# Kernel optimization log

Hardware: AMD Instinct MI355X
Metric: run time of the kernel (lower is better)

## Reference

```python
import jax, jax.numpy as jnp
import numpy as np

# Static options from the deep-stabilization repo
WIDTH, HEIGHT = 1920.0, 1080.0
NUM_GRID_ROWS = 12
FOV = 0.8  # virtual-camera vertical field of view (radians)


def quat_to_rotmat(q):
    """Quaternion (x, y, z, w) -> rotation matrix; q: [..., 4] -> [..., 3, 3]."""
    q = q / jnp.linalg.norm(q, axis=-1, keepdims=True)
    x, y, z, w = q[..., 0], q[..., 1], q[..., 2], q[..., 3]
    R = jnp.stack([
        1 - 2 * (y * y + z * z), 2 * (x * y - z * w), 2 * (x * z + y * w),
        2 * (x * y + z * w), 1 - 2 * (x * x + z * z), 2 * (y * z - x * w),
        2 * (x * z - y * w), 2 * (y * z + x * w), 1 - 2 * (x * x + y * y)
    ], axis=-1)
    return R.reshape(q.shape[:-1] + (3, 3))


def intrinsics():
    f = 0.5 * HEIGHT / np.tan(0.5 * FOV)
    return jnp.array([[f, 0.0, 0.5 * WIDTH],
                      [0.0, f, 0.5 * HEIGHT],
                      [0.0, 0.0, 1.0]], dtype=jnp.float32)


def setup_inputs() -> dict:
    key = jax.random.key(0)
    k1, k2 = jax.random.split(key)
    B = 1_048_576
    # Virtual camera quaternions [B, 4]
    Vt = jax.random.normal(k1, (B, 4), dtype=jnp.float32)
    # Real projections per grid row: K @ R(q) so they are valid, well-conditioned
    # projection matrices [B, NUM_GRID_ROWS, 3, 3]
    q = jax.random.normal(k2, (B, NUM_GRID_ROWS, 4), dtype=jnp.float32)
    Rr = quat_to_rotmat(q)
    real_projection_t = jnp.einsum('ij,brjk->brik', intrinsics(), Rr)
    return {"Vt": Vt, "real_projection_t": real_projection_t}


def reference(Vt, real_projection_t):
    K = intrinsics()
    # Virtual projection: K @ R(quat)  -> [B, 3, 3]
    Pv = jnp.einsum('ij,bjk->bik', K, quat_to_rotmat(Vt))
    # Real projection at the middle grid row -> [B, 3, 3]
    Pr = real_projection_t[:, NUM_GRID_ROWS // 2]
    # Homography from virtual frame to real frame
    transform = jnp.matmul(Pr, jnp.linalg.inv(Pv))  # [B, 3, 3]

    x0, x1 = int(WIDTH * 0.1), int(WIDTH * 0.9)
    y0, y1 = int(HEIGHT * 0.1), int(HEIGHT * 0.9)
    corners = jnp.array([[x0, y0, 1.0], [x0, y1, 1.0],
                         [x1, y0, 1.0], [x1, y1, 1.0]], dtype=jnp.float32)  # [4,3]

    pts = jnp.einsum('bij,cj->bci', transform, corners)  # [B, 4, 3]
    pts = pts / pts[..., 2:3]                            # homogeneous normalize
    xy = pts[..., :2] / jnp.array([WIDTH, HEIGHT], dtype=jnp.float32)  # [B,4,2]

    # Piecewise penalty |d|: d = x if x<0, 1-x if x>1, else 0  =>  relu(-x)+relu(x-1)
    viol = jax.nn.relu(-xy) + jax.nn.relu(xy - 1.0)  # [B, 4, 2]
    per_corner = viol.sum(axis=-1)                   # [B, 4]
    loss = per_corner.max(axis=-1).sum()             # max over corners, sum over batch
    return loss.reshape(1)
```

## Files before the change

kernel.cpp:

```cpp
#include <hip/hip_runtime.h>
#include <cmath>


__global__ __launch_bounds__(256) void loss_kernel(
    const float* __restrict__ Vt,
    const float* __restrict__ Prt,
    float* __restrict__ out,
    int B,
    float d0x, float d0y, float d1x, float d1y,
    float d2x, float d2y, float d3x, float d3y)
{
    int b = blockIdx.x * blockDim.x + threadIdx.x;
    float loss = 0.0f;
    if (b < B) {
        float4 q4 = *reinterpret_cast<const float4*>(Vt + 4ll * b);
        float qx = q4.x, qy = q4.y, qz = q4.z, qw = q4.w;
        float n  = sqrtf(qx*qx + qy*qy + qz*qz + qw*qw);
        float in_ = 1.0f / n;
        qx *= in_; qy *= in_; qz *= in_; qw *= in_;
        float r00 = 1.0f - 2.0f*(qy*qy + qz*qz);
        float r01 = 2.0f*(qx*qy - qz*qw);
        float r02 = 2.0f*(qx*qz + qy*qw);
        float r10 = 2.0f*(qx*qy + qz*qw);
        float r11 = 1.0f - 2.0f*(qx*qx + qz*qz);
        float r12 = 2.0f*(qy*qz - qx*qw);
        float r20 = 2.0f*(qx*qz - qy*qw);
        float r21 = 2.0f*(qy*qz + qx*qw);
        float r22 = 1.0f - 2.0f*(qx*qx + qy*qy);

        const float* P = Prt + (size_t)b * 108 + 54;
        float2 a0 = *reinterpret_cast<const float2*>(P + 0);
        float2 a1 = *reinterpret_cast<const float2*>(P + 2);
        float2 a2 = *reinterpret_cast<const float2*>(P + 4);
        float2 a3 = *reinterpret_cast<const float2*>(P + 6);
        float  p8 = P[8];
        float P0=a0.x, P1=a0.y, P2=a1.x, P3=a1.y, P4=a2.x, P5=a2.y, P6=a3.x, P7=a3.y, P8=p8;

        float m00 = P0*r00 + P1*r01 + P2*r02;
        float m01 = P0*r10 + P1*r11 + P2*r12;
        float m02 = P0*r20 + P1*r21 + P2*r22;
        float m10 = P3*r00 + P4*r01 + P5*r02;
        float m11 = P3*r10 + P4*r11 + P5*r12;
        float m12 = P3*r20 + P4*r21 + P5*r22;
        float m20 = P6*r00 + P7*r01 + P8*r02;
        float m21 = P6*r10 + P7*r11 + P8*r12;
        float m22 = P6*r20 + P7*r21 + P8*r22;

        const float invW = 1.0f / 1920.0f, invH = 1.0f / 1080.0f;
        float best = -1e30f;
        float dxs[4] = {d0x, d1x, d2x, d3x};
        float dys[4] = {d0y, d1y, d2y, d3y};
        #pragma unroll
        for (int c = 0; c < 4; ++c) {
            float dx = dxs[c], dy = dys[c];
            float px = m00*dx + m01*dy + m02;
            float py = m10*dx + m11*dy + m12;
            float pz = m20*dx + m21*dy + m22;
            float rz = 1.0f / pz;
            float x  = px * rz * invW;
            float y  = py * rz * invH;
            float v  = fmaxf(0.0f, -x) + fmaxf(0.0f, x - 1.0f)
                     + fmaxf(0.0f, -y) + fmaxf(0.0f, y - 1.0f);
            best = fmaxf(best, v);
        }
        loss = best;
    }

    #pragma unroll
    for (int off = 32; off > 0; off >>= 1)
        loss += __shfl_down(loss, off, 64);
    __shared__ float smem[4];
    int lane = threadIdx.x & 63;
    int wv   = threadIdx.x >> 6;
    if (lane == 0) smem[wv] = loss;
    __syncthreads();
    if (threadIdx.x == 0) {
        float s = smem[0] + smem[1] + smem[2] + smem[3];
        atomicAdd(out, s);
    }
}

extern "C" void kernel_launch(void* const* d_in, const int* in_sizes, int n_in,
                              void* d_out, int out_size, void* d_ws, size_t ws_size,
                              hipStream_t stream) {
    const float* Vt  = (const float*)d_in[0];
    const float* Prt = (const float*)d_in[1];
    float* out = (float*)d_out;
    int B = in_sizes[0] / 4;

    const double fd = 0.5 * 1080.0 / tan(0.5 * 0.8);
    const float  f  = (float)fd;
    const float  cx = 0.5f * 1920.0f, cy = 0.5f * 1080.0f;
    const float  x0 = 192.0f, x1 = 1728.0f, y0 = 108.0f, y1 = 972.0f;
    float d0x = (x0 - cx) / f, d0y = (y0 - cy) / f;
    float d1x = (x0 - cx) / f, d1y = (y1 - cy) / f;
    float d2x = (x1 - cx) / f, d2y = (y0 - cy) / f;
    float d3x = (x1 - cx) / f, d3y = (y1 - cy) / f;

    hipMemsetAsync(d_out, 0, sizeof(float), stream);
    int threads = 256;
    int blocks  = (B + threads - 1) / threads;
    loss_kernel<<<blocks, threads, 0, stream>>>(Vt, Prt, out, B,
        d0x, d0y, d1x, d1y, d2x, d2y, d3x, d3y);
}
```

Baseline: 531.5 us.

## Stage middle-row projections through LDS with coalesced aligned float4 loads

Each block of 256 records now loads the 16-byte-aligned 64-byte sections that contain the middle-row 3x3 matrices. It does this for groups of 4 records using cooperative float4 loads, writes them into a padded shared-memory stage, and each thread then reads its 9 floats from LDS at a fixed offset. The goal is to replace the strided, unaligned float2/float loads from a 432-byte record stride with fewer, wider, better-coalesced memory transactions. The cost is extra LDS traffic and a barrier, and a tail path that falls back to direct global loads for partial blocks.

```diff
diff --git a/kernel.cpp b/kernel.cpp
--- a/kernel.cpp
+++ b/kernel.cpp
@@ -1,6 +1,56 @@
 #include <hip/hip_runtime.h>
 #include <cmath>
 
+
+__device__ __forceinline__ float record_loss(
+    float qx, float qy, float qz, float qw, const float* __restrict__ P,
+    float d0x, float d0y, float d1x, float d1y,
+    float d2x, float d2y, float d3x, float d3y)
+{
+    float n  = sqrtf(qx*qx + qy*qy + qz*qz + qw*qw);
+    float in_ = 1.0f / n;
+    qx *= in_; qy *= in_; qz *= in_; qw *= in_;
+    float r00 = 1.0f - 2.0f*(qy*qy + qz*qz);
+    float r01 = 2.0f*(qx*qy - qz*qw);
+    float r02 = 2.0f*(qx*qz + qy*qw);
+    float r10 = 2.0f*(qx*qy + qz*qw);
+    float r11 = 1.0f - 2.0f*(qx*qx + qz*qz);
+    float r12 = 2.0f*(qy*qz - qx*qw);
+    float r20 = 2.0f*(qx*qz - qy*qw);
+    float r21 = 2.0f*(qy*qz + qx*qw);
+    float r22 = 1.0f - 2.0f*(qx*qx + qy*qy);
+
+    float P0=P[0],P1=P[1],P2=P[2],P3=P[3],P4=P[4],P5=P[5],P6=P[6],P7=P[7],P8=P[8];
+
+    float m00 = P0*r00 + P1*r01 + P2*r02;
+    float m01 = P0*r10 + P1*r11 + P2*r12;
+    float m02 = P0*r20 + P1*r21 + P2*r22;
+    float m10 = P3*r00 + P4*r01 + P5*r02;
+    float m11 = P3*r10 + P4*r11 + P5*r12;
+    float m12 = P3*r20 + P4*r21 + P5*r22;
+    float m20 = P6*r00 + P7*r01 + P8*r02;
+    float m21 = P6*r10 + P7*r11 + P8*r12;
+    float m22 = P6*r20 + P7*r21 + P8*r22;
+
+    const float invW = 1.0f / 1920.0f, invH = 1.0f / 1080.0f;
+    float best = -1e30f;
+    float dxs[4] = {d0x, d1x, d2x, d3x};
+    float dys[4] = {d0y, d1y, d2y, d3y};
+    #pragma unroll
+    for (int c = 0; c < 4; ++c) {
+        float dx = dxs[c], dy = dys[c];
+        float px = m00*dx + m01*dy + m02;
+        float py = m10*dx + m11*dy + m12;
+        float pz = m20*dx + m21*dy + m22;
+        float rz = 1.0f / pz;
+        float x  = px * rz * invW;
+        float y  = py * rz * invH;
+        float v  = fmaxf(0.0f, -x) + fmaxf(0.0f, x - 1.0f)
+                 + fmaxf(0.0f, -y) + fmaxf(0.0f, y - 1.0f);
+        best = fmaxf(best, v);
+    }
+    return best;
+}
 
 __global__ __launch_bounds__(256) void loss_kernel(
     const float* __restrict__ Vt,
@@ -10,72 +60,58 @@
     float d0x, float d0y, float d1x, float d1y,
     float d2x, float d2y, float d3x, float d3y)
 {
-    int b = blockIdx.x * blockDim.x + threadIdx.x;
+    __shared__ float stage[64 * 100];
+    __shared__ float wsum[4];
+
+    const int t = threadIdx.x;
+    const long long R = (long long)blockIdx.x * 256;
     float loss = 0.0f;
-    if (b < B) {
-        float4 q4 = *reinterpret_cast<const float4*>(Vt + 4ll * b);
-        float qx = q4.x, qy = q4.y, qz = q4.z, qw = q4.w;
-        float n  = sqrtf(qx*qx + qy*qy + qz*qz + qw*qw);
-        float in_ = 1.0f / n;
-        qx *= in_; qy *= in_; qz *= in_; qw *= in_;
-        float r00 = 1.0f - 2.0f*(qy*qy + qz*qz);
-        float r01 = 2.0f*(qx*qy - qz*qw);
-        float r02 = 2.0f*(qx*qz + qy*qw);
-        float r10 = 2.0f*(qx*qy + qz*qw);
-        float r11 = 1.0f - 2.0f*(qx*qx + qz*qz);
-        float r12 = 2.0f*(qy*qz - qx*qw);
-        float r20 = 2.0f*(qx*qz - qy*qw);
-        float r21 = 2.0f*(qy*qz + qx*qw);
-        float r22 = 1.0f - 2.0f*(qx*qx + qy*qy);
 
-        const float* P = Prt + (size_t)b * 108 + 54;
-        float2 a0 = *reinterpret_cast<const float2*>(P + 0);
-        float2 a1 = *reinterpret_cast<const float2*>(P + 2);
-        float2 a2 = *reinterpret_cast<const float2*>(P + 4);
-        float2 a3 = *reinterpret_cast<const float2*>(P + 6);
-        float  p8 = P[8];
-        float P0=a0.x, P1=a0.y, P2=a1.x, P3=a1.y, P4=a2.x, P5=a2.y, P6=a3.x, P7=a3.y, P8=p8;
+    if (R + 256 <= (long long)B) {
+        const char* base = (const char*)Prt;
+        const int secoff[6] = {192, 640, 1024, 1088, 1472, 1536};
+        #pragma unroll
+        for (int i = 0; i < 6; ++i) {
+            int c   = i * 256 + t;
+            int g   = c / 24;
+            int rem = c - g * 24;
+            int s   = rem >> 2;
+            int q   = rem & 3;
+            long long gaddr = (R + 4ll * g) * 432 + secoff[s] + q * 16;
+            float4 v = *reinterpret_cast<const float4*>(base + gaddr);
+            *reinterpret_cast<float4*>(stage + g * 100 + s * 16 + q * 4) = v;
+        }
+        float4 q4 = *reinterpret_cast<const float4*>(Vt + 4 * (R + t));
+        __syncthreads();
 
-        float m00 = P0*r00 + P1*r01 + P2*r02;
-        float m01 = P0*r10 + P1*r11 + P2*r12;
-        float m02 = P0*r20 + P1*r21 + P2*r22;
-        float m10 = P3*r00 + P4*r01 + P5*r02;
-        float m11 = P3*r10 + P4*r11 + P5*r12;
-        float m12 = P3*r20 + P4*r21 + P5*r22;
-        float m20 = P6*r00 + P7*r01 + P8*r02;
-        float m21 = P6*r10 + P7*r11 + P8*r12;
-        float m22 = P6*r20 + P7*r21 + P8*r22;
-
-        const float invW = 1.0f / 1920.0f, invH = 1.0f / 1080.0f;
-        float best = -1e30f;
-        float dxs[4] = {d0x, d1x, d2x, d3x};
-        float dys[4] = {d0y, d1y, d2y, d3y};
-        #pragma unroll
-        for (int c = 0; c < 4; ++c) {
-            float dx = dxs[c], dy = dys[c];
-            float px = m00*dx + m01*dy + m02;
-            float py = m10*dx + m11*dy + m12;
-            float pz = m20*dx + m21*dy + m22;
-            float rz = 1.0f / pz;
-            float x  = px * rz * invW;
-            float y  = py * rz * invH;
-            float v  = fmaxf(0.0f, -x) + fmaxf(0.0f, x - 1.0f)
-                     + fmaxf(0.0f, -y) + fmaxf(0.0f, y - 1.0f);
-            best = fmaxf(best, v);
+        const int g = t >> 2, j = t & 3;
+        const int foff[4] = {6, 18, 46, 74};
+        const float* P = stage + g * 100 + foff[j];
+        loss = record_loss(q4.x, q4.y, q4.z, q4.w, P,
+                           d0x, d0y, d1x, d1y, d2x, d2y, d3x, d3y);
+    } else {
+        long long b = R + t;
+        if (b < B) {
+            float4 q4 = *reinterpret_cast<const float4*>(Vt + 4 * b);
+            float Pl[9];
+            const float* P = Prt + (size_t)b * 108 + 54;
+            #pragma unroll
+            for (int k = 0; k < 9; ++k) Pl[k] = P[k];
+            loss = record_loss(q4.x, q4.y, q4.z, q4.w, Pl,
+                               d0x, d0y, d1x, d1y, d2x, d2y, d3x, d3y);
         }
-        loss = best;
+        __syncthreads();
     }
 
     #pragma unroll
     for (int off = 32; off > 0; off >>= 1)
         loss += __shfl_down(loss, off, 64);
-    __shared__ float smem[4];
-    int lane = threadIdx.x & 63;
-    int wv   = threadIdx.x >> 6;
-    if (lane == 0) smem[wv] = loss;
+    int lane = t & 63;
+    int wv   = t >> 6;
+    if (lane == 0) wsum[wv] = loss;
     __syncthreads();
-    if (threadIdx.x == 0) {
-        float s = smem[0] + smem[1] + smem[2] + smem[3];
+    if (t == 0) {
+        float s = wsum[0] + wsum[1] + wsum[2] + wsum[3];
         atomicAdd(out, s);
     }
 }
```

Result: no change. 535.8 us (+0.8%).
